# Kernel optimization log

Hardware: AMD Instinct MI355X
Metric: run time of the kernel (lower is better)

## Reference

```python
import jax, jax.numpy as jnp
import numpy as np

HIDDEN = 1024
HEADS = 16
HEAD_DIM = HIDDEN // HEADS
FF = 4 * HIDDEN
B, S = 2, 2048


def _linear_params(key, out_dim, in_dim):
    kw, kb = jax.random.split(key)
    bound = 1.0 / np.sqrt(in_dim)
    W = jax.random.uniform(kw, (out_dim, in_dim), jnp.float32, -bound, bound)
    b = jax.random.uniform(kb, (out_dim,), jnp.float32, -bound, bound)
    return W, b


def setup_inputs() -> dict:
    key = jax.random.key(0)
    ks = jax.random.split(key, 8)
    x = jax.random.normal(ks[0], (B, S, HIDDEN), jnp.float32)
    attention_mask = jnp.ones((B, S), jnp.float32)
    Wq, bq = _linear_params(ks[1], HIDDEN, HIDDEN)
    Wk, bk = _linear_params(ks[2], HIDDEN, HIDDEN)
    Wv, bv = _linear_params(ks[3], HIDDEN, HIDDEN)
    Wo, bo = _linear_params(ks[4], HIDDEN, HIDDEN)
    W1, b1 = _linear_params(ks[5], FF, HIDDEN)
    W2, b2 = _linear_params(ks[6], HIDDEN, FF)
    g1 = jnp.ones((HIDDEN,), jnp.float32); be1 = jnp.zeros((HIDDEN,), jnp.float32)
    g2 = jnp.ones((HIDDEN,), jnp.float32); be2 = jnp.zeros((HIDDEN,), jnp.float32)
    return dict(x=x, attention_mask=attention_mask,
                Wq=Wq, bq=bq, Wk=Wk, bk=bk, Wv=Wv, bv=bv, Wo=Wo, bo=bo,
                W1=W1, b1=b1, W2=W2, b2=b2,
                g1=g1, be1=be1, g2=g2, be2=be2)


def _layer_norm(x, g, b, eps=1e-5):
    mu = jnp.mean(x, axis=-1, keepdims=True)
    var = jnp.mean(jnp.square(x - mu), axis=-1, keepdims=True)
    return (x - mu) * jax.lax.rsqrt(var + eps) * g + b


def reference(x, attention_mask, Wq, bq, Wk, bk, Wv, bv, Wo, bo,
              W1, b1, W2, b2, g1, be1, g2, be2):
    # Dropout is identity (eval mode / deterministic reference).
    residual = x
    h = _layer_norm(x, g1, be1)
    # [B,S,H] -> [B,nH,S,dh]
    def heads(t):
        return t.reshape(B, S, HEADS, HEAD_DIM).transpose(0, 2, 1, 3)
    q = heads(h @ Wq.T + bq)
    k = heads(h @ Wk.T + bk)
    v = heads(h @ Wv.T + bv)
    scores = jnp.einsum('bhqd,bhkd->bhqk', q, k) / np.sqrt(HEAD_DIM).astype(np.float32)
    scores = scores + (attention_mask[:, None, None, :] - 1.0) * 10000.0
    attn = jax.nn.softmax(scores, axis=-1)
    ctx = jnp.einsum('bhqk,bhkd->bhqd', attn, v)
    ctx = ctx.transpose(0, 2, 1, 3).reshape(B, S, HIDDEN)
    attn_out = ctx @ Wo.T + bo
    x = residual + attn_out
    residual = x
    h = _layer_norm(x, g2, be2)
    h = jax.nn.gelu(h @ W1.T + b1, approximate=False)
    h = h @ W2.T + b2
    return residual + h
```

## Files before the change

kernel.cpp:

```cpp
#include <hip/hip_runtime.h>
#include <hip/hip_bf16.h>
#include <math.h>

typedef __bf16 bf16;
typedef __bf16 bf16x2 __attribute__((ext_vector_type(2)));
typedef __bf16 bf16x4v __attribute__((ext_vector_type(4)));
typedef __bf16 bf16x8 __attribute__((ext_vector_type(8)));
typedef float  f32x4  __attribute__((ext_vector_type(4)));
typedef unsigned u32x4 __attribute__((ext_vector_type(4)));
typedef unsigned u32x2 __attribute__((ext_vector_type(2)));

#define HIDDEN 1024
#define TOKENS 4096
#define FFDIM  4096
#define SEQ    2048
#define NHEAD  16

#define LOG2E 1.44269504088896340736f

__device__ __forceinline__ void async_copy16(bf16* lds, const bf16* g)
{
    __builtin_amdgcn_global_load_lds(
        (__attribute__((address_space(1))) void*)g,
        (__attribute__((address_space(3))) void*)lds,
        16, 0, 0);
}

__device__ __forceinline__ unsigned pack2(float lo, float hi)
{
    bf16x2 t; t[0] = (bf16)lo; t[1] = (bf16)hi;
    return __builtin_bit_cast(unsigned, t);
}

__device__ __forceinline__ void pl32swap(unsigned& a, unsigned& b)
{
    u32x2 r = __builtin_amdgcn_permlane32_swap(a, b, false, false);
    a = r.x; b = r.y;
}

__device__ __forceinline__ float gelu_fast(float v)
{
    float x = fabsf(v) * 0.70710678118654752f;
    float t = __builtin_amdgcn_rcpf(1.0f + 0.3275911f * x);
    float p = t * (0.254829592f + t * (-0.284496736f + t * (1.421413741f + t * (-1.453152027f + t * 1.061405429f))));
    float e = __builtin_amdgcn_exp2f(-x * x * LOG2E);
    float erfv = 1.0f - p * e;
    erfv = (v < 0.0f) ? -erfv : erfv;
    return 0.5f * v * (1.0f + erfv);
}

__global__ __launch_bounds__(256) void cvt_all_kernel(const float* __restrict__ wq,
    const float* __restrict__ wk, const float* __restrict__ wv, const float* __restrict__ wo,
    const float* __restrict__ w1, const float* __restrict__ w2, bf16* __restrict__ out)
{
    size_t i = ((size_t)blockIdx.x * 256 + threadIdx.x) * 4;
    int sel = (int)(i >> 20);
    const float* src;
    size_t off;
    if (sel < 4) { src = (sel == 0) ? wq : (sel == 1) ? wk : (sel == 2) ? wv : wo; off = i & ((1u << 20) - 1); }
    else if (sel < 8) { src = w1; off = i - ((size_t)4 << 20); }
    else              { src = w2; off = i - ((size_t)8 << 20); }
    float4 v = *(const float4*)&src[off];
    bf16x4v o = { (bf16)v.x, (bf16)v.y, (bf16)v.z, (bf16)v.w };
    *(bf16x4v*)&out[i] = o;
}

__global__ __launch_bounds__(256) void concat_bias_kernel(const float* __restrict__ bq,
    const float* __restrict__ bk, const float* __restrict__ bv, float* __restrict__ o)
{
    int i = blockIdx.x * 256 + threadIdx.x;
    float v = (i < 1024) ? bq[i] : (i < 2048 ? bk[i - 1024] : bv[i - 2048]);
    o[i] = v;
}

__global__ __launch_bounds__(256) void ln_kernel(const float* __restrict__ in,
    const float* __restrict__ g, const float* __restrict__ be, bf16* __restrict__ out)
{
    int row = blockIdx.x;
    int tid = threadIdx.x;
    const float* x = in + (size_t)row * HIDDEN;
    int i0 = tid * 4;
    float4 v = *(const float4*)&x[i0];
    float s  = v.x + v.y + v.z + v.w;
    float s2 = v.x*v.x + v.y*v.y + v.z*v.z + v.w*v.w;
    #pragma unroll
    for (int off = 32; off > 0; off >>= 1) { s += __shfl_xor(s, off); s2 += __shfl_xor(s2, off); }
    __shared__ float red[2][4];
    int wave = tid >> 6;
    if ((tid & 63) == 0) { red[0][wave] = s; red[1][wave] = s2; }
    __syncthreads();
    float ts  = red[0][0] + red[0][1] + red[0][2] + red[0][3];
    float ts2 = red[1][0] + red[1][1] + red[1][2] + red[1][3];
    float mu   = ts  * (1.0f / HIDDEN);
    float var  = ts2 * (1.0f / HIDDEN) - mu * mu;
    float rstd = rsqrtf(var + 1e-5f);
    float4 gg = *(const float4*)&g[i0];
    float4 bb = *(const float4*)&be[i0];
    bf16x4v o;
    o[0] = (bf16)((v.x - mu) * rstd * gg.x + bb.x);
    o[1] = (bf16)((v.y - mu) * rstd * gg.y + bb.y);
    o[2] = (bf16)((v.z - mu) * rstd * gg.z + bb.z);
    o[3] = (bf16)((v.w - mu) * rstd * gg.w + bb.w);
    *(bf16x4v*)&out[(size_t)row * HIDDEN + i0] = o;
}

template<int BM, int EPI, typename OT>
__global__ __launch_bounds__(256) void gemm_bt(const bf16* __restrict__ A, const bf16* __restrict__ Bt,
    const float* __restrict__ bias, const float* __restrict__ res, OT* __restrict__ C,
    int M, int N, int K)
{
    constexpr int MT = BM / 32;
    __shared__ bf16 As[BM * 64];
    __shared__ bf16 Bs[128 * 64];
    int tid  = threadIdx.x;
    int wave = tid >> 6, lane = tid & 63;
    int lm = lane & 15, quad = lane >> 4;
    int m0 = blockIdx.x * BM, n0 = blockIdx.y * 128;
    int wm = (wave >> 1) * (MT * 16), wn = (wave & 1) * 64;
    int r8 = lane >> 3, c8 = lane & 7;
    int gsw = (c8 ^ (r8 & 7)) * 8;
    f32x4 acc[MT][4] = {};
    for (int k0 = 0; k0 < K; k0 += 64) {
        #pragma unroll
        for (int ch = wave; ch < BM / 8; ch += 4)
            async_copy16(As + ch * 512, &A[(size_t)(m0 + ch * 8 + r8) * K + k0 + gsw]);
        #pragma unroll
        for (int ch = wave; ch < 16; ch += 4)
            async_copy16(Bs + ch * 512, &Bt[(size_t)(n0 + ch * 8 + r8) * K + k0 + gsw]);
        __syncthreads();
        bf16x8 af[MT][2], bfr[4][2];
        #pragma unroll
        for (int ks = 0; ks < 2; ks++) {
            int co = ((ks * 4 + quad) ^ (lm & 7)) * 8;
            #pragma unroll
            for (int t = 0; t < MT; t++) af[t][ks]  = *(const bf16x8*)&As[(wm + t * 16 + lm) * 64 + co];
            #pragma unroll
            for (int t = 0; t < 4; t++)  bfr[t][ks] = *(const bf16x8*)&Bs[(wn + t * 16 + lm) * 64 + co];
        }
        #pragma unroll
        for (int mt = 0; mt < MT; mt++)
            #pragma unroll
            for (int nt = 0; nt < 4; nt++)
                #pragma unroll
                for (int ks = 0; ks < 2; ks++)
                    acc[mt][nt] = __builtin_amdgcn_mfma_f32_16x16x32_bf16(af[mt][ks], bfr[nt][ks], acc[mt][nt], 0, 0, 0);
        __syncthreads();
    }
    #pragma unroll
    for (int mt = 0; mt < MT; mt++) {
        #pragma unroll
        for (int nt = 0; nt < 4; nt++) {
            int col = n0 + wn + nt * 16 + lm;
            float bv = bias[col];
            #pragma unroll
            for (int r = 0; r < 4; r++) {
                int row = m0 + wm + mt * 16 + quad * 4 + r;
                float vv = acc[mt][nt][r] + bv;
                if (EPI == 1) vv = gelu_fast(vv);
                if (EPI == 2) vv += res[(size_t)row * N + col];
                C[(size_t)row * N + col] = (OT)vv;
            }
        }
    }
}

__global__ __launch_bounds__(256) void gemm_qkv(const bf16* __restrict__ A, const bf16* __restrict__ W,
    const float* __restrict__ bias, bf16* __restrict__ qb, bf16* __restrict__ kb, bf16* __restrict__ vt)
{
    constexpr int K = HIDDEN;
    __shared__ bf16 As[128 * 64];
    __shared__ bf16 Bs[128 * 64];
    int tid  = threadIdx.x;
    int wave = tid >> 6, lane = tid & 63;
    int lm = lane & 15, quad = lane >> 4;
    int m0 = blockIdx.x * 128, n0 = blockIdx.y * 128;
    int wm = (wave >> 1) * 64, wn = (wave & 1) * 64;
    int r8 = lane >> 3, c8 = lane & 7;
    int gsw = (c8 ^ (r8 & 7)) * 8;
    f32x4 acc[4][4] = {};
    for (int k0 = 0; k0 < K; k0 += 64) {
        #pragma unroll
        for (int ch = wave; ch < 16; ch += 4) {
            async_copy16(As + ch * 512, &A[(size_t)(m0 + ch * 8 + r8) * K + k0 + gsw]);
            async_copy16(Bs + ch * 512, &W[(size_t)(n0 + ch * 8 + r8) * K + k0 + gsw]);
        }
        __syncthreads();
        bf16x8 af[4][2], bfr[4][2];
        #pragma unroll
        for (int ks = 0; ks < 2; ks++) {
            int co = ((ks * 4 + quad) ^ (lm & 7)) * 8;
            #pragma unroll
            for (int t = 0; t < 4; t++) {
                af[t][ks]  = *(const bf16x8*)&As[(wm + t * 16 + lm) * 64 + co];
                bfr[t][ks] = *(const bf16x8*)&Bs[(wn + t * 16 + lm) * 64 + co];
            }
        }
        #pragma unroll
        for (int mt = 0; mt < 4; mt++)
            #pragma unroll
            for (int nt = 0; nt < 4; nt++)
                #pragma unroll
                for (int ks = 0; ks < 2; ks++)
                    acc[mt][nt] = __builtin_amdgcn_mfma_f32_16x16x32_bf16(af[mt][ks], bfr[nt][ks], acc[mt][nt], 0, 0, 0);
        __syncthreads();
    }
    int region = n0 >> 10;
    #pragma unroll
    for (int mt = 0; mt < 4; mt++) {
        #pragma unroll
        for (int nt = 0; nt < 4; nt++) {
            int col = n0 + wn + nt * 16 + lm;
            float bv = bias[col];
            int cl = col & 1023;
            #pragma unroll
            for (int r = 0; r < 4; r++) {
                int row = m0 + wm + mt * 16 + quad * 4 + r;
                float vv = acc[mt][nt][r] + bv;
                if (region == 0)      qb[(size_t)row * HIDDEN + cl] = (bf16)vv;
                else if (region == 1) kb[(size_t)row * HIDDEN + cl] = (bf16)vv;
                else {
                    int h = cl >> 6, d = cl & 63;
                    int b = row >> 11, s = row & 2047;
                    vt[(((size_t)(b * NHEAD + h)) * 64 + d) * SEQ + s] = (bf16)vv;
                }
            }
        }
    }
}

__global__ __launch_bounds__(512, 4) void attn_kernel(const bf16* __restrict__ Q, const bf16* __restrict__ K,
    const bf16* __restrict__ Vt, const float* __restrict__ mask, bf16* __restrict__ O)
{
    __shared__ bf16 smem[32768];
    int tid = threadIdx.x, wave = tid >> 6, lane = tid & 63;
    int lm = lane & 15, quad = lane >> 4;
    int pair = wave >> 1, h = wave & 1;
    int bh = blockIdx.y, b = bh >> 4;
    int q0 = blockIdx.x * 128 + pair * 32;
    const size_t base  = ((size_t)b * SEQ) * HIDDEN + (bh & 15) * 64;
    const size_t vbase = (size_t)bh * 64 * SEQ;
    int srow8 = lane >> 3, spos = lane & 7;
    bf16x8 qf[2][2];
    #pragma unroll
    for (int qt = 0; qt < 2; qt++)
        #pragma unroll
        for (int ks = 0; ks < 2; ks++)
            qf[qt][ks] = *(const bf16x8*)&Q[base + (size_t)(q0 + qt * 16 + lm) * HIDDEN + ks * 32 + quad * 8];
    bf16x8 onesf;
    #pragma unroll
    for (int i = 0; i < 8; i++) onesf[i] = (bf16)1.0f;
    f32x4 o[2][4] = {};
    f32x4 lacc[2] = {};
    const float c0 = 0.125f * LOG2E;
    const float cmk = 10000.0f * LOG2E;
    const float coff = -(cmk + 16.0f);
    int r = wave * 8 + srow8;
    int gc = spos ^ (r & 7);
    auto stage = [&](int gbuf, int ktg) {
        #pragma unroll
        for (int s = 0; s < 2; s++) {
            bf16* kd = smem + ((gbuf << 1) + s) * 4096;
            bf16* vd = smem + 16384 + ((gbuf << 1) + s) * 4096;
            int kt = ktg + s * 64;
            async_copy16(kd + wave * 512, &K [base  + (size_t)(kt + r) * HIDDEN + gc * 8]);
            async_copy16(vd + wave * 512, &Vt[vbase + (size_t)r * SEQ + kt + gc * 8]);
        }
    };
    stage(0, 0);
    int kh = h * 32;
    bool qodd = (quad & 1);
    for (int gi = 0; gi < SEQ / 128; gi++) {
        __syncthreads();
        if (gi + 1 < SEQ / 128) stage((gi + 1) & 1, (gi + 1) * 128);
        #pragma unroll
        for (int sub = 0; sub < 2; sub++) {
            const bf16* ksb = smem + (((gi & 1) << 1) + sub) * 4096;
            const bf16* vsb = smem + 16384 + (((gi & 1) << 1) + sub) * 4096;
            int kt = gi * 128 + sub * 64;
            bf16x8 kf[2][2];
            #pragma unroll
            for (int nt = 0; nt < 2; nt++)
                #pragma unroll
                for (int ks = 0; ks < 2; ks++)
                    kf[nt][ks] = *(const bf16x8*)&ksb[(kh + nt * 16 + lm) * 64 + (((ks * 4 + quad) ^ (lm & 7)) * 8)];
            f32x4 st[2][2] = {};
            #pragma unroll
            for (int qt = 0; qt < 2; qt++)
                #pragma unroll
                for (int nt = 0; nt < 2; nt++)
                    #pragma unroll
                    for (int ks = 0; ks < 2; ks++)
                        st[qt][nt] = __builtin_amdgcn_mfma_f32_16x16x32_bf16(kf[nt][ks], qf[qt][ks], st[qt][nt], 0, 0, 0);
            float madd[2][4];
            #pragma unroll
            for (int nt = 0; nt < 2; nt++) {
                float4 mv = *(const float4*)&mask[b * SEQ + kt + kh + nt * 16 + quad * 4];
                madd[nt][0] = mv.x * cmk + coff; madd[nt][1] = mv.y * cmk + coff;
                madd[nt][2] = mv.z * cmk + coff; madd[nt][3] = mv.w * cmk + coff;
            }
            bf16x8 af[2];
            #pragma unroll
            for (int qt = 0; qt < 2; qt++) {
                unsigned w[2][2];
                #pragma unroll
                for (int nt = 0; nt < 2; nt++) {
                    float p0 = __builtin_amdgcn_exp2f(st[qt][nt][0] * c0 + madd[nt][0]);
                    float p1 = __builtin_amdgcn_exp2f(st[qt][nt][1] * c0 + madd[nt][1]);
                    float p2 = __builtin_amdgcn_exp2f(st[qt][nt][2] * c0 + madd[nt][2]);
                    float p3 = __builtin_amdgcn_exp2f(st[qt][nt][3] * c0 + madd[nt][3]);
                    w[nt][0] = pack2(p0, p1);
                    w[nt][1] = pack2(p2, p3);
                }
                unsigned A0 = w[0][0], B0 = w[1][0];
                unsigned A1 = w[0][1], B1 = w[1][1];
                pl32swap(A0, B0);
                pl32swap(A1, B1);
                unsigned F0 = __shfl_xor(A0, 16), G0 = __shfl_xor(B0, 16);
                unsigned F1 = __shfl_xor(A1, 16), G1 = __shfl_xor(B1, 16);
                u32x4 uu;
                uu.x = qodd ? G0 : A0;
                uu.y = qodd ? G1 : A1;
                uu.z = qodd ? B0 : F0;
                uu.w = qodd ? B1 : F1;
                af[qt] = __builtin_bit_cast(bf16x8, uu);
                lacc[qt] = __builtin_amdgcn_mfma_f32_16x16x32_bf16(af[qt], onesf, lacc[qt], 0, 0, 0);
            }
            #pragma unroll
            for (int dt = 0; dt < 4; dt++) {
                bf16x8 vf = *(const bf16x8*)&vsb[(dt * 16 + lm) * 64 + (((4 * h + quad) ^ (lm & 7)) * 8)];
                #pragma unroll
                for (int qt = 0; qt < 2; qt++)
                    o[qt][dt] = __builtin_amdgcn_mfma_f32_16x16x32_bf16(af[qt], vf, o[qt][dt], 0, 0, 0);
            }
        }
    }
    __syncthreads();
    float* scratch = (float*)smem;
    float* s = scratch + ((size_t)pair * 64 + lane) * 20;
    if (h == 1) {
        #pragma unroll
        for (int dt = 0; dt < 4; dt++) *(f32x4*)&s[dt * 4] = o[0][dt];
        *(f32x4*)&s[16] = lacc[0];
    }
    __syncthreads();
    if (h == 0) {
        f32x4 pl = *(const f32x4*)&s[16];
        #pragma unroll
        for (int rr = 0; rr < 4; rr++) {
            float inv = 1.0f / (lacc[0][rr] + pl[rr]);
            #pragma unroll
            for (int dt = 0; dt < 4; dt++) {
                float val = (o[0][dt][rr] + s[dt * 4 + rr]) * inv;
                O[base + (size_t)(q0 + quad * 4 + rr) * HIDDEN + dt * 16 + lm] = (bf16)val;
            }
        }
    }
    __syncthreads();
    if (h == 0) {
        #pragma unroll
        for (int dt = 0; dt < 4; dt++) *(f32x4*)&s[dt * 4] = o[1][dt];
        *(f32x4*)&s[16] = lacc[1];
    }
    __syncthreads();
    if (h == 1) {
        f32x4 pl = *(const f32x4*)&s[16];
        #pragma unroll
        for (int rr = 0; rr < 4; rr++) {
            float inv = 1.0f / (lacc[1][rr] + pl[rr]);
            #pragma unroll
            for (int dt = 0; dt < 4; dt++) {
                float val = (o[1][dt][rr] + s[dt * 4 + rr]) * inv;
                O[base + (size_t)(q0 + 16 + quad * 4 + rr) * HIDDEN + dt * 16 + lm] = (bf16)val;
            }
        }
    }
}

extern "C" void kernel_launch(void* const* d_in, const int* in_sizes, int n_in,
                              void* d_out, int out_size, void* d_ws, size_t ws_size,
                              hipStream_t stream)
{
    (void)in_sizes; (void)n_in; (void)out_size; (void)ws_size;
    const float* x    = (const float*)d_in[0];
    const float* mask = (const float*)d_in[1];
    const float* Wq   = (const float*)d_in[2];
    const float* bq   = (const float*)d_in[3];
    const float* Wk   = (const float*)d_in[4];
    const float* bk   = (const float*)d_in[5];
    const float* Wv   = (const float*)d_in[6];
    const float* bv   = (const float*)d_in[7];
    const float* Wo   = (const float*)d_in[8];
    const float* bo   = (const float*)d_in[9];
    const float* W1   = (const float*)d_in[10];
    const float* b1   = (const float*)d_in[11];
    const float* W2   = (const float*)d_in[12];
    const float* b2   = (const float*)d_in[13];
    const float* g1   = (const float*)d_in[14];
    const float* be1  = (const float*)d_in[15];
    const float* g2   = (const float*)d_in[16];
    const float* be2  = (const float*)d_in[17];
    float* out = (float*)d_out;

    const size_t M1 = 1024u * 1024u;
    bf16* ws    = (bf16*)d_ws;
    bf16* Wqkv_b = ws;
    bf16* Wo_b  = ws + 3 * M1;
    bf16* W1_b  = ws + 4 * M1;
    bf16* W2_b  = ws + 8 * M1;
    bf16* qb    = ws + 12 * M1;
    bf16* kb    = ws + 16 * M1;
    bf16* vt    = ws + 20 * M1;
    bf16* cx    = ws + 24 * M1;
    bf16* h     = ws + 28 * M1;
    bf16* ffb   = ws + 12 * M1;
    float* biasqkv = (float*)(ws + 24 * M1);

    cvt_all_kernel<<<dim3(12288), 256, 0, stream>>>(Wq, Wk, Wv, Wo, W1, W2, Wqkv_b);
    concat_bias_kernel<<<dim3(12), 256, 0, stream>>>(bq, bk, bv, biasqkv);

    ln_kernel<<<dim3(TOKENS), 256, 0, stream>>>(x, g1, be1, h);
    gemm_qkv<<<dim3(32, 24), 256, 0, stream>>>(h, Wqkv_b, biasqkv, qb, kb, vt);
    attn_kernel<<<dim3(SEQ / 128, 32), 512, 0, stream>>>(qb, kb, vt, mask, cx);
    gemm_bt<64, 2, float><<<dim3(64, 8), 256, 0, stream>>>(cx, Wo_b, bo, x, out, TOKENS, HIDDEN, HIDDEN);
    ln_kernel<<<dim3(TOKENS), 256, 0, stream>>>(out, g2, be2, h);
    gemm_bt<128, 1, bf16><<<dim3(32, 32), 256, 0, stream>>>(h, W1_b, b1, nullptr, ffb, TOKENS, FFDIM, HIDDEN);
    gemm_bt<64, 2, float><<<dim3(64, 8), 256, 0, stream>>>(ffb, W2_b, b2, out, out, TOKENS, HIDDEN, FFDIM);
}
```

Baseline: 371.3 us.

## Double-buffer LDS tiles in GEMM kernels to overlap loads with MFMA

Both GEMM kernels get two LDS buffers for the A and B tiles. The async global-to-LDS copy of the next K-tile is issued right after the barrier, so it runs while MFMAs work on the current tile, and the trailing barrier per iteration is removed. The aim is to hide global load latency behind compute. In exchange, LDS use per block doubles (64KB for the 128-row tiles), which may lower occupancy.

```diff
diff --git a/kernel.cpp b/kernel.cpp
--- a/kernel.cpp
+++ b/kernel.cpp
@@ -110,8 +110,8 @@
     int M, int N, int K)
 {
     constexpr int MT = BM / 32;
-    __shared__ bf16 As[BM * 64];
-    __shared__ bf16 Bs[128 * 64];
+    __shared__ bf16 As[2][BM * 64];
+    __shared__ bf16 Bs[2][128 * 64];
     int tid  = threadIdx.x;
     int wave = tid >> 6, lane = tid & 63;
     int lm = lane & 15, quad = lane >> 4;
@@ -119,23 +119,30 @@
     int wm = (wave >> 1) * (MT * 16), wn = (wave & 1) * 64;
     int r8 = lane >> 3, c8 = lane & 7;
     int gsw = (c8 ^ (r8 & 7)) * 8;
+    auto stage = [&](int buf, int k0) {
+        #pragma unroll
+        for (int ch = wave; ch < BM / 8; ch += 4)
+            async_copy16(&As[buf][ch * 512], &A[(size_t)(m0 + ch * 8 + r8) * K + k0 + gsw]);
+        #pragma unroll
+        for (int ch = wave; ch < 16; ch += 4)
+            async_copy16(&Bs[buf][ch * 512], &Bt[(size_t)(n0 + ch * 8 + r8) * K + k0 + gsw]);
+    };
     f32x4 acc[MT][4] = {};
-    for (int k0 = 0; k0 < K; k0 += 64) {
-        #pragma unroll
-        for (int ch = wave; ch < BM / 8; ch += 4)
-            async_copy16(As + ch * 512, &A[(size_t)(m0 + ch * 8 + r8) * K + k0 + gsw]);
-        #pragma unroll
-        for (int ch = wave; ch < 16; ch += 4)
-            async_copy16(Bs + ch * 512, &Bt[(size_t)(n0 + ch * 8 + r8) * K + k0 + gsw]);
+    stage(0, 0);
+    int nk = K >> 6;
+    for (int t = 0; t < nk; t++) {
         __syncthreads();
+        if (t + 1 < nk) stage((t + 1) & 1, (t + 1) * 64);
+        const bf16* as = As[t & 1];
+        const bf16* bs = Bs[t & 1];
         bf16x8 af[MT][2], bfr[4][2];
         #pragma unroll
         for (int ks = 0; ks < 2; ks++) {
             int co = ((ks * 4 + quad) ^ (lm & 7)) * 8;
             #pragma unroll
-            for (int t = 0; t < MT; t++) af[t][ks]  = *(const bf16x8*)&As[(wm + t * 16 + lm) * 64 + co];
-            #pragma unroll
-            for (int t = 0; t < 4; t++)  bfr[t][ks] = *(const bf16x8*)&Bs[(wn + t * 16 + lm) * 64 + co];
+            for (int t2 = 0; t2 < MT; t2++) af[t2][ks]  = *(const bf16x8*)&as[(wm + t2 * 16 + lm) * 64 + co];
+            #pragma unroll
+            for (int t2 = 0; t2 < 4; t2++)  bfr[t2][ks] = *(const bf16x8*)&bs[(wn + t2 * 16 + lm) * 64 + co];
         }
         #pragma unroll
         for (int mt = 0; mt < MT; mt++)
@@ -144,7 +151,6 @@
                 #pragma unroll
                 for (int ks = 0; ks < 2; ks++)
                     acc[mt][nt] = __builtin_amdgcn_mfma_f32_16x16x32_bf16(af[mt][ks], bfr[nt][ks], acc[mt][nt], 0, 0, 0);
-        __syncthreads();
     }
     #pragma unroll
     for (int mt = 0; mt < MT; mt++) {
@@ -168,8 +174,8 @@
     const float* __restrict__ bias, bf16* __restrict__ qb, bf16* __restrict__ kb, bf16* __restrict__ vt)
 {
     constexpr int K = HIDDEN;
-    __shared__ bf16 As[128 * 64];
-    __shared__ bf16 Bs[128 * 64];
+    __shared__ bf16 As[2][128 * 64];
+    __shared__ bf16 Bs[2][128 * 64];
     int tid  = threadIdx.x;
     int wave = tid >> 6, lane = tid & 63;
     int lm = lane & 15, quad = lane >> 4;
@@ -177,22 +183,29 @@
     int wm = (wave >> 1) * 64, wn = (wave & 1) * 64;
     int r8 = lane >> 3, c8 = lane & 7;
     int gsw = (c8 ^ (r8 & 7)) * 8;
+    auto stage = [&](int buf, int k0) {
+        #pragma unroll
+        for (int ch = wave; ch < 16; ch += 4) {
+            async_copy16(&As[buf][ch * 512], &A[(size_t)(m0 + ch * 8 + r8) * K + k0 + gsw]);
+            async_copy16(&Bs[buf][ch * 512], &W[(size_t)(n0 + ch * 8 + r8) * K + k0 + gsw]);
+        }
+    };
     f32x4 acc[4][4] = {};
-    for (int k0 = 0; k0 < K; k0 += 64) {
-        #pragma unroll
-        for (int ch = wave; ch < 16; ch += 4) {
-            async_copy16(As + ch * 512, &A[(size_t)(m0 + ch * 8 + r8) * K + k0 + gsw]);
-            async_copy16(Bs + ch * 512, &W[(size_t)(n0 + ch * 8 + r8) * K + k0 + gsw]);
-        }
+    stage(0, 0);
+    constexpr int nk = K >> 6;
+    for (int t = 0; t < nk; t++) {
         __syncthreads();
+        if (t + 1 < nk) stage((t + 1) & 1, (t + 1) * 64);
+        const bf16* as = As[t & 1];
+        const bf16* bs = Bs[t & 1];
         bf16x8 af[4][2], bfr[4][2];
         #pragma unroll
         for (int ks = 0; ks < 2; ks++) {
             int co = ((ks * 4 + quad) ^ (lm & 7)) * 8;
             #pragma unroll
-            for (int t = 0; t < 4; t++) {
-                af[t][ks]  = *(const bf16x8*)&As[(wm + t * 16 + lm) * 64 + co];
-                bfr[t][ks] = *(const bf16x8*)&Bs[(wn + t * 16 + lm) * 64 + co];
+            for (int t2 = 0; t2 < 4; t2++) {
+                af[t2][ks]  = *(const bf16x8*)&as[(wm + t2 * 16 + lm) * 64 + co];
+                bfr[t2][ks] = *(const bf16x8*)&bs[(wn + t2 * 16 + lm) * 64 + co];
             }
         }
         #pragma unroll
@@ -202,7 +215,6 @@
                 #pragma unroll
                 for (int ks = 0; ks < 2; ks++)
                     acc[mt][nt] = __builtin_amdgcn_mfma_f32_16x16x32_bf16(af[mt][ks], bfr[nt][ks], acc[mt][nt], 0, 0, 0);
-        __syncthreads();
     }
     int region = n0 >> 10;
     #pragma unroll
```

Measured after the change: 355.7 us. 1.04x faster.
